# Kernel optimization log

Hardware: AMD Instinct MI355X
Metric: run time of the kernel (lower is better)

Reference implementation:

```python
import jax, jax.numpy as jnp
import numpy as np

N_SITES, NODE_F = 50000, 64
N_PERM, N_NEIGH = 12, 8
IN_F = N_NEIGH * NODE_F  # 512
OUT_F = 64
LN2 = float(np.log(2.0))


def setup_inputs() -> dict:
    key = jax.random.key(0)
    k1, k2, k3, k4 = jax.random.split(key, 4)
    X_sites = jax.random.normal(k1, (N_SITES, NODE_F), dtype=jnp.float32)
    X_NSs = jax.random.randint(k2, (N_SITES, N_PERM, N_NEIGH), 0, N_SITES)
    # nn.Linear(IN_F, OUT_F): weight (OUT_F, IN_F), bias (OUT_F,)
    bound = 1.0 / np.sqrt(IN_F)
    W = jax.random.uniform(k3, (OUT_F, IN_F), minval=-bound, maxval=bound, dtype=jnp.float32)
    b = jax.random.uniform(k4, (OUT_F,), minval=-bound, maxval=bound, dtype=jnp.float32)
    return {"X_sites": X_sites, "X_NSs": X_NSs, "W": W, "b": b}


def reference(X_sites, X_NSs, W, b):
    # Gather neighbor features: (N, P, K, F) -> (N, P, K*F)
    gathered = X_sites[X_NSs].reshape(X_NSs.shape[0], N_PERM, IN_F)
    # Linear: (N, P, IN_F) @ (IN_F, OUT_F) + b
    x1 = jnp.einsum('npi,oi->npo', gathered, W) + b
    # Shifted softplus: softplus(x) - log(2)  (dropout treated as identity / eval mode)
    x2 = jax.nn.softplus(x1) - LN2
    # Sum over permutations -> (N, OUT_F)
    return x2.sum(axis=1)
```

## Files before the change

kernel.cpp:

```cpp
#include <hip/hip_runtime.h>
#include <hip/hip_bf16.h>

#define N_SITES 50000
#define N_PERM  12
#define N_NEIGH 8
#define NODE_F  64
#define IN_F    512
#define OUT_F   64
#define N_TILES (N_SITES / 16)
#define LN2F    0.69314718055994530942f

#define XCHUNKS (N_SITES * NODE_F / 8)
#define WCHUNKS (OUT_F * IN_F / 8)
#define SLOT_E  520
#define BUF_E   (16 * SLOT_E)

typedef __bf16 bf16x8 __attribute__((ext_vector_type(8)));
typedef float  f32x4  __attribute__((ext_vector_type(4)));

__device__ __forceinline__ unsigned short f32_to_bf16_rne(unsigned int u) {
    u += 0x7FFFu + ((u >> 16) & 1u);
    return (unsigned short)(u >> 16);
}

__device__ __forceinline__ int probe_is_bf16(const void* Xorig) {
    int lane = threadIdx.x & 63;
    unsigned short h = ((const unsigned short*)Xorig)[2 * lane];
    int e = (h >> 7) & 0xFF;
    unsigned long long mm = __ballot(e >= 110 && e <= 140);
    return (__popcll(mm) >= 48) ? 1 : 0;
}

__device__ __forceinline__ void pack8(const uint4* src, uint4* dst, int c) {
    uint4 a = src[2 * c], b = src[2 * c + 1];
    uint4 o;
    o.x = (unsigned int)f32_to_bf16_rne(a.x) | ((unsigned int)f32_to_bf16_rne(a.y) << 16);
    o.y = (unsigned int)f32_to_bf16_rne(a.z) | ((unsigned int)f32_to_bf16_rne(a.w) << 16);
    o.z = (unsigned int)f32_to_bf16_rne(b.x) | ((unsigned int)f32_to_bf16_rne(b.y) << 16);
    o.w = (unsigned int)f32_to_bf16_rne(b.z) | ((unsigned int)f32_to_bf16_rne(b.w) << 16);
    dst[c] = o;
}

__global__ void convert_all(const void* __restrict__ Xv, const void* __restrict__ Wv,
                            const void* __restrict__ Bv, uint4* __restrict__ Xb,
                            uint4* __restrict__ Wb, float* __restrict__ Bf) {
    const int isbf = probe_is_bf16(Xv);
    int c = blockIdx.x * blockDim.x + threadIdx.x;
    if (c < XCHUNKS) {
        if (isbf) Xb[c] = ((const uint4*)Xv)[c];
        else      pack8((const uint4*)Xv, Xb, c);
    } else if (c < XCHUNKS + WCHUNKS) {
        int cw = c - XCHUNKS;
        if (isbf) Wb[cw] = ((const uint4*)Wv)[cw];
        else      pack8((const uint4*)Wv, Wb, cw);
    } else if (c < XCHUNKS + WCHUNKS + OUT_F) {
        int i = c - XCHUNKS - WCHUNKS;
        Bf[i] = isbf ? (float)((const __bf16*)Bv)[i] : ((const float*)Bv)[i];
    }
}

__device__ __forceinline__ float softplus_sh(float x) {
    float t = __expf(-fabsf(x));
    return fmaxf(x, 0.f) + 0.69314718056f * __log2f(1.f + t);
}

__device__ __forceinline__ void async16(const __bf16* g, __bf16* l) {
    __builtin_amdgcn_global_load_lds(
        (const __attribute__((address_space(1))) unsigned int*)g,
        (__attribute__((address_space(3))) unsigned int*)l, 16, 0, 0);
}

__global__ __launch_bounds__(256, 2)
void lcnn_dma(const void* __restrict__ Xorig, const __bf16* __restrict__ Xb,
              const int* __restrict__ NS, const __bf16* __restrict__ Wb,
              const float* __restrict__ Bf, void* __restrict__ outv)
{
    __shared__ __align__(16) __bf16 Abuf[2][BUF_E];

    const int wave = threadIdx.x >> 6;
    const int lane = threadIdx.x & 63;
    const int m    = lane & 15;
    const int quad = lane >> 4;
    const int mk   = m & 7;
    const int mh   = m >> 3;
    const int tile = blockIdx.x;

    bf16x8 Wfrag[16];
    #pragma unroll
    for (int ks = 0; ks < 16; ++ks)
        Wfrag[ks] = *(const bf16x8*)(Wb + (size_t)(wave * 16 + m) * IN_F + ks * 32 + quad * 8);

    const float bias = Bf[wave * 16 + m];

    auto load_idx = [&](int p_, int out[4]) {
        #pragma unroll
        for (int i = 0; i < 4; ++i) {
            int t = wave * 4 + i;
            int s = ((t & 1) << 3) + (lane >> 3);
            int k = t >> 1;
            out[i] = NS[(size_t)(tile * 16 + s) * (N_PERM * N_NEIGH) + p_ * N_NEIGH + k];
        }
    };
    auto stage = [&](int buf_, const int idxv[4]) {
        const int csrc = (lane & 7) ^ (lane >> 3);
        #pragma unroll
        for (int i = 0; i < 4; ++i) {
            int t = wave * 4 + i;
            async16(Xb + (size_t)idxv[i] * NODE_F + csrc * 8, &Abuf[buf_][t * SLOT_E]);
        }
    };

    int idxn[4];
    load_idx(0, idxn);
    stage(0, idxn);
    load_idx(1, idxn);
    __syncthreads();

    f32x4 sum = {0.f, 0.f, 0.f, 0.f};
    for (int p = 0; p < N_PERM; ++p) {
        if (p < N_PERM - 1) stage((p + 1) & 1, idxn);
        if (p < N_PERM - 2) load_idx(p + 2, idxn);

        f32x4 acc = {0.f, 0.f, 0.f, 0.f};
        const __bf16* bb = &Abuf[p & 1][0];
        #pragma unroll
        for (int ks = 0; ks < 16; ++ks) {
            int t_r = (ks >> 1) * 2 + mh;
            int j   = ((ks & 1) << 2) | quad;
            bf16x8 afr = *(const bf16x8*)(bb + t_r * SLOT_E + mk * 64 + ((j ^ mk) << 3));
            acc = __builtin_amdgcn_mfma_f32_16x16x32_bf16(afr, Wfrag[ks], acc, 0, 0, 0);
        }
        #pragma unroll
        for (int r = 0; r < 4; ++r) sum[r] += softplus_sh(acc[r] + bias);
        __syncthreads();
    }

    const int isbf = probe_is_bf16(Xorig);
    #pragma unroll
    for (int r = 0; r < 4; ++r) {
        size_t pos = (size_t)(tile * 16 + quad * 4 + r) * OUT_F + wave * 16 + m;
        float v = sum[r] - 12.0f * LN2F;
        if (isbf) ((__bf16*)outv)[pos] = (__bf16)v;
        else      ((float*)outv)[pos]  = v;
    }
}

__global__ void lcnn_fallback(const float* __restrict__ X, const int* __restrict__ NS,
                              const float* __restrict__ W, const float* __restrict__ B,
                              float* __restrict__ out) {
    int t = blockIdx.x * blockDim.x + threadIdx.x;
    if (t >= N_SITES * OUT_F) return;
    int sitei = t >> 6, o = t & 63;
    const int* ns = NS + (size_t)sitei * 96;
    float s = 0.f;
    for (int p = 0; p < N_PERM; ++p) {
        float x = B[o];
        for (int n = 0; n < N_NEIGH; ++n) {
            const float* xr = X + (size_t)ns[p * 8 + n] * NODE_F;
            const float* wr = W + (size_t)o * IN_F + n * NODE_F;
            for (int f = 0; f < NODE_F; ++f) x += xr[f] * wr[f];
        }
        s += softplus_sh(x);
    }
    out[t] = s - 12.0f * LN2F;
}

extern "C" void kernel_launch(void* const* d_in, const int* in_sizes, int n_in,
                              void* d_out, int out_size, void* d_ws, size_t ws_size,
                              hipStream_t stream) {
    const void* X  = d_in[0];
    const int*  NS = (const int*)d_in[1];
    const void* W  = d_in[2];
    const void* B  = d_in[3];

    char* ws = (char*)d_ws;
    __bf16* Xb = (__bf16*)ws;
    __bf16* Wb = (__bf16*)(ws + (size_t)XCHUNKS * 16);
    float*  Bf = (float*)(ws + (size_t)(XCHUNKS + WCHUNKS) * 16);
    const bool conv = ws_size >= (size_t)(XCHUNKS + WCHUNKS) * 16 + OUT_F * 4;

    if (conv) {
        int nch = XCHUNKS + WCHUNKS + OUT_F;
        hipLaunchKernelGGL(convert_all, dim3((nch + 255) / 256), dim3(256), 0, stream,
                           X, W, B, (uint4*)Xb, (uint4*)Wb, Bf);
        hipLaunchKernelGGL(lcnn_dma, dim3(N_TILES), dim3(256), 0, stream,
                           X, Xb, NS, Wb, Bf, d_out);
    } else {
        hipLaunchKernelGGL(lcnn_fallback,
                           dim3((N_SITES * OUT_F + 255) / 256), dim3(256), 0, stream,
                           (const float*)X, NS, (const float*)W, (const float*)B,
                           (float*)d_out);
    }
}
```

Measured before the change: 146.1 us.

## Triple-buffer gathered tiles with partial vmcnt waits and preload all indices

Switches the LDS staging from double to triple buffering, so the async gather for permutation p+2 is issued while p is computed. The per-iteration barrier becomes a raw s_barrier that waits only for older loads (vmcnt(4)). All 12 permutations' neighbor indices are loaded into registers up front, and the loop is fully unrolled. Launch bounds go to 3 waves per SIMD. The cost is more LDS per block and more registers, which may limit occupancy.

```diff
diff --git a/kernel.cpp b/kernel.cpp
--- a/kernel.cpp
+++ b/kernel.cpp
@@ -70,12 +70,19 @@
         (__attribute__((address_space(3))) unsigned int*)l, 16, 0, 0);
 }
 
-__global__ __launch_bounds__(256, 2)
+
+#define BARX(N) do {                                                          \
+        asm volatile("s_waitcnt vmcnt(" #N ") lgkmcnt(0)" ::: "memory");      \
+        __builtin_amdgcn_s_barrier();                                         \
+        asm volatile("" ::: "memory");                                        \
+    } while (0)
+
+__global__ __launch_bounds__(256, 3)
 void lcnn_dma(const void* __restrict__ Xorig, const __bf16* __restrict__ Xb,
               const int* __restrict__ NS, const __bf16* __restrict__ Wb,
               const float* __restrict__ Bf, void* __restrict__ outv)
 {
-    __shared__ __align__(16) __bf16 Abuf[2][BUF_E];
+    __shared__ __align__(16) __bf16 Abuf[3][BUF_E];
 
     const int wave = threadIdx.x >> 6;
     const int lane = threadIdx.x & 63;
@@ -92,37 +99,36 @@
 
     const float bias = Bf[wave * 16 + m];
 
-    auto load_idx = [&](int p_, int out[4]) {
-        #pragma unroll
-        for (int i = 0; i < 4; ++i) {
-            int t = wave * 4 + i;
-            int s = ((t & 1) << 3) + (lane >> 3);
-            int k = t >> 1;
-            out[i] = NS[(size_t)(tile * 16 + s) * (N_PERM * N_NEIGH) + p_ * N_NEIGH + k];
-        }
+    const int srow = lane >> 3;
+    const int csrc = (lane & 7) ^ srow;
+    const int* ns0 = NS + (size_t)(tile * 16 + srow)     * (N_PERM * N_NEIGH) + wave * 2;
+    const int* ns1 = NS + (size_t)(tile * 16 + srow + 8) * (N_PERM * N_NEIGH) + wave * 2;
+
+    int4 idx[N_PERM];
+    #pragma unroll
+    for (int p = 0; p < N_PERM; ++p) {
+        idx[p].x = ns0[p * N_NEIGH];     idx[p].y = ns1[p * N_NEIGH];
+        idx[p].z = ns0[p * N_NEIGH + 1]; idx[p].w = ns1[p * N_NEIGH + 1];
+    }
+
+    auto stagep = [&](int bslot, int4 iv) {
+        async16(Xb + (size_t)iv.x * NODE_F + csrc * 8, &Abuf[bslot][(wave * 4 + 0) * SLOT_E]);
+        async16(Xb + (size_t)iv.y * NODE_F + csrc * 8, &Abuf[bslot][(wave * 4 + 1) * SLOT_E]);
+        async16(Xb + (size_t)iv.z * NODE_F + csrc * 8, &Abuf[bslot][(wave * 4 + 2) * SLOT_E]);
+        async16(Xb + (size_t)iv.w * NODE_F + csrc * 8, &Abuf[bslot][(wave * 4 + 3) * SLOT_E]);
     };
-    auto stage = [&](int buf_, const int idxv[4]) {
-        const int csrc = (lane & 7) ^ (lane >> 3);
-        #pragma unroll
-        for (int i = 0; i < 4; ++i) {
-            int t = wave * 4 + i;
-            async16(Xb + (size_t)idxv[i] * NODE_F + csrc * 8, &Abuf[buf_][t * SLOT_E]);
-        }
-    };
-
-    int idxn[4];
-    load_idx(0, idxn);
-    stage(0, idxn);
-    load_idx(1, idxn);
-    __syncthreads();
+
+    stagep(0, idx[0]);
+    stagep(1, idx[1]);
+    BARX(4);
 
     f32x4 sum = {0.f, 0.f, 0.f, 0.f};
+    #pragma unroll
     for (int p = 0; p < N_PERM; ++p) {
-        if (p < N_PERM - 1) stage((p + 1) & 1, idxn);
-        if (p < N_PERM - 2) load_idx(p + 2, idxn);
+        if (p < N_PERM - 2) stagep((p + 2) % 3, idx[p + 2]);
 
         f32x4 acc = {0.f, 0.f, 0.f, 0.f};
-        const __bf16* bb = &Abuf[p & 1][0];
+        const __bf16* bb = &Abuf[p % 3][0];
         #pragma unroll
         for (int ks = 0; ks < 16; ++ks) {
             int t_r = (ks >> 1) * 2 + mh;
@@ -132,7 +138,9 @@
         }
         #pragma unroll
         for (int r = 0; r < 4; ++r) sum[r] += softplus_sh(acc[r] + bias);
-        __syncthreads();
+
+        if (p < N_PERM - 2)      BARX(4);
+        else if (p < N_PERM - 1) BARX(0);
     }
 
     const int isbf = probe_is_bf16(Xorig);
```

After: 141.9 us, median of 2. 2.9% less time.
